# Kernel tuning notes

Measured on AMD Instinct MI355X. Metric: run time of the kernel, lower is better.

Reference implementation:

```python
import jax, jax.numpy as jnp
import numpy as np

SCORE_THR = 0.01
IOU_THR = 0.1          # NOTE: original layer hardcodes 0.1 in tf.image.non_max_suppression
MAX_DET = 100
NEG = jnp.float32(-1e30)


def _iou_one_vs_all(box, boxes):
    # box: [4] (y1,x1,y2,x2), boxes: [N,4]
    y1 = jnp.maximum(box[0], boxes[:, 0])
    x1 = jnp.maximum(box[1], boxes[:, 1])
    y2 = jnp.minimum(box[2], boxes[:, 2])
    x2 = jnp.minimum(box[3], boxes[:, 3])
    inter = jnp.maximum(y2 - y1, 0.0) * jnp.maximum(x2 - x1, 0.0)
    a = (box[2] - box[0]) * (box[3] - box[1])
    b = (boxes[:, 2] - boxes[:, 0]) * (boxes[:, 3] - boxes[:, 1])
    return inter / (a + b - inter + 1e-8)


def _nms_keep(boxes, scores):
    # Greedy NMS as a keep-mask over N anchors. Matches tf.image.non_max_suppression
    # restricted to anchors with score > SCORE_THR, up to MAX_DET selections.
    s = jnp.where(scores > SCORE_THR, scores, NEG)
    keep0 = jnp.zeros(s.shape, dtype=bool)

    def step(carry, _):
        s, keep = carry
        i = jnp.argmax(s)
        ok = s[i] > NEG * 0.5
        keep = keep.at[i].set(ok)
        iou = _iou_one_vs_all(boxes[i], boxes)
        s = jnp.where((iou > IOU_THR) & ok, NEG, s)
        s = s.at[i].set(NEG)
        return (s, keep), None

    (_, keep), _ = jax.lax.scan(step, (s, keep0), None, length=MAX_DET)
    return keep


def _filter_image(boxes_i, cls_i):
    # boxes_i: [N,4], cls_i: [N,C]
    C = cls_i.shape[1]
    # class-specific NMS: keep mask per class -> [C, N]
    keep = jax.vmap(lambda s: _nms_keep(boxes_i, s))(cls_i.T)
    keep_flat = keep.T.reshape(-1)          # [N*C], (anchor, class) flat order
    flat = cls_i.reshape(-1)                # [N*C]
    masked = jnp.where(keep_flat, flat, NEG)
    vals, idx = jax.lax.top_k(masked, MAX_DET)
    valid = vals > NEG * 0.5
    anchor = idx // C
    label = idx % C
    scores_out = jnp.where(valid, jnp.take(flat, idx), -1.0)
    boxes_out = jnp.where(valid[:, None], boxes_i[anchor], -1.0)
    labels_out = jnp.where(valid, label, -1).astype(jnp.int32)
    return boxes_out, scores_out, labels_out


def setup_inputs() -> dict:
    key = jax.random.key(0)
    k1, k2, k3 = jax.random.split(key, 3)
    B, N, C = 4, 49104, 90
    yx1 = jax.random.uniform(k1, (B, N, 2), dtype=jnp.float32) * 512.0
    hw = jax.random.uniform(k2, (B, N, 2), dtype=jnp.float32) * 128.0 + 1.0
    boxes = jnp.concatenate([yx1, yx1 + hw], axis=-1)          # [B,N,4] y1x1y2x2
    classification = jax.random.uniform(k3, (B, N, C), dtype=jnp.float32)
    return {"boxes": boxes, "classification": classification}


def reference(boxes, classification):
    return jax.vmap(_filter_image)(boxes, classification)
```

## Files before the change

kernel.cpp:

```cpp
#include <hip/hip_runtime.h>
#include <stdint.h>

typedef unsigned long long u64;

#define B_ 4
#define N_ 49104
#define C_ 90
#define NCLS (B_ * C_)
#define MAXK 100
#define THR 0.01f
#define NB2 2048
#define KCAP 640
#define PTGT 448
#define PCAP 512
#define ACH 128
#define NCH ((N_ + ACH - 1) / ACH)
#define CAPC 32
#define NBIN_M 1280
#define BINBASE 0x3F6E0000u
#define BINSH_M 10

__device__ __forceinline__ float area_of(float y1, float x1, float y2, float x2) {
#pragma clang fp contract(off)
  return (y2 - y1) * (x2 - x1);
}

#define IOU_MID (26843547.0 / 268435456.0)

__device__ __forceinline__ bool iou_gt(float ay1, float ax1, float ay2, float ax2, float aa,
                                       float by1, float bx1, float by2, float bx2, float ba) {
#pragma clang fp contract(off)
  float y1 = fmaxf(ay1, by1);
  float x1 = fmaxf(ax1, bx1);
  float y2 = fminf(ay2, by2);
  float x2 = fminf(ax2, bx2);
  float inter = fmaxf(y2 - y1, 0.0f) * fmaxf(x2 - x1, 0.0f);
  float denom = aa + ba - inter + 1e-8f;
  return (double)inter >= IOU_MID * (double)denom;
}

__device__ __forceinline__ u64 umax64(u64 a, u64 b) { return a > b ? a : b; }

__device__ __forceinline__ u64 shfl_xor_u64(u64 v, int m) {
  int lo = __shfl_xor((int)(unsigned)v, m);
  int hi = __shfl_xor((int)(unsigned)(v >> 32), m);
  return ((u64)(unsigned)hi << 32) | (u64)(unsigned)lo;
}

__device__ __forceinline__ int key2bin_m(u64 k) {
  int d = (int)((unsigned)(k >> 32) - BINBASE);
  int bin = d >> BINSH_M;
  if (d < 0) bin = 0;
  if (bin > NBIN_M - 1) bin = NBIN_M - 1;
  return bin;
}

__global__ __launch_bounds__(256) void select_kernel(const float* __restrict__ cls,
                                                     u64* __restrict__ keybuf,
                                                     unsigned* __restrict__ cnt,
                                                     int capsel, float t0) {
  __shared__ u64 ll[C_ * CAPC];
  __shared__ unsigned lcnt[C_];
  __shared__ unsigned base_s[C_];
  int blk = blockIdx.x;
  int b = blk / NCH, ch = blk - b * NCH;
  int a0 = ch * ACH;
  int aEnd = a0 + ACH; if (aEnd > N_) aEnd = N_;
  int e0 = a0 * C_;
  int nelem = (aEnd - a0) * C_;
  int tid = threadIdx.x;

  for (int i = tid; i < C_; i += 256) lcnt[i] = 0u;
  __syncthreads();

  const float4* src4 = (const float4*)(cls + (size_t)b * N_ * C_ + e0);
  int n4 = nelem >> 2;
  for (int i4 = tid; i4 < n4; i4 += 256) {
    float4 v = src4[i4];
#pragma unroll
    for (int j = 0; j < 4; ++j) {
      float s = (&v.x)[j];
      if (s > t0) {
        int e = e0 + i4 * 4 + j;
        unsigned n = (unsigned)e / (unsigned)C_;
        unsigned c = (unsigned)e - n * (unsigned)C_;
        u64 key = ((u64)__float_as_uint(s) << 32) | (u64)(0xFFFFFFFFu - n);
        unsigned pos = atomicAdd(&lcnt[c], 1u);
        if (pos < CAPC) {
          ll[c * CAPC + pos] = key;
        } else {
          unsigned g = (unsigned)(b * C_) + c;
          unsigned gp = atomicAdd(&cnt[g * 16], 1u);
          if (gp < (unsigned)capsel) keybuf[(size_t)g * capsel + gp] = key;
        }
      }
    }
  }
  __syncthreads();

  if (tid < C_) {
    unsigned cc = lcnt[tid]; if (cc > CAPC) cc = CAPC;
    base_s[tid] = atomicAdd(&cnt[(b * C_ + tid) * 16], cc);
  }
  __syncthreads();

  for (int i = tid; i < C_ * CAPC; i += 256) {
    int c = i >> 5, j = i & 31;
    unsigned cc = lcnt[c]; if (cc > CAPC) cc = CAPC;
    if ((unsigned)j < cc) {
      unsigned pos = base_s[c] + (unsigned)j;
      if (pos < (unsigned)capsel)
        keybuf[(size_t)(b * C_ + c) * capsel + pos] = ll[i];
    }
  }
}

__global__ __launch_bounds__(512) void nms_kernel(const float* __restrict__ boxes,
                                                  const float* __restrict__ cls,
                                                  const u64* __restrict__ keybuf,
                                                  const unsigned* __restrict__ cnt,
                                                  unsigned* __restrict__ done,
                                                  int capsel, float t0,
                                                  u64* __restrict__ keepkeys,
                                                  int* __restrict__ nk_arr,
                                                  float* __restrict__ out) {
  int gcls = blockIdx.x;
  int b = gcls / C_, c = gcls - b * C_;
  __shared__ u64 karr[KCAP];
  __shared__ unsigned hist[NB2];
  __shared__ unsigned sfx[NB2];
  __shared__ float4 kb[MAXK];
  __shared__ float ka[MAXK];
  __shared__ unsigned wsum[8];
  __shared__ int sh_cnt[8];
  __shared__ int sh_b1, sh_pl;
  __shared__ int sh_last, sh_thr;
  __shared__ unsigned sh_cc;
  int tid = threadIdx.x;
  int lane = tid & 63;
  int wid = tid >> 6;

  for (int i = tid; i < MAXK; i += 512) keepkeys[(size_t)gcls * MAXK + i] = 0ull;
  for (int i = tid; i < NB2; i += 512) hist[i] = 0u;
  if (tid == 0) sh_b1 = -1;
  __syncthreads();

  unsigned Mraw = cnt[gcls * 16];
  bool overflow = (Mraw > (unsigned)capsel);
  int M = overflow ? 0 : (int)Mraw;

  const u64* src = keybuf + (size_t)gcls * capsel;

  const int PK = 4096 / 512;
  u64 kreg[PK];
#pragma unroll
  for (int q = 0; q < PK; ++q) {
    kreg[q] = 0ull;
    int i = q * 512 + tid;
    if (i < M) {
      kreg[q] = src[i];
      atomicAdd(&hist[(unsigned)(kreg[q] >> 44) & (NB2 - 1)], 1u);
    }
  }
  __syncthreads();

  {
    const int W = NB2 / 512;
    unsigned loc[W];
    unsigned psum = 0;
#pragma unroll
    for (int q = 0; q < W; ++q) {
      psum += hist[NB2 - 1 - (tid * W + q)];
      loc[q] = psum;
    }
    unsigned incl = psum;
#pragma unroll
    for (int s = 1; s < 64; s <<= 1) {
      unsigned v = (unsigned)__shfl_up((int)incl, s);
      if (lane >= s) incl += v;
    }
    if (lane == 63) wsum[wid] = incl;
    __syncthreads();
    unsigned bs = incl - psum;
    for (int w2 = 0; w2 < wid; ++w2) bs += wsum[w2];
#pragma unroll
    for (int q = 0; q < W; ++q)
      sfx[NB2 - 1 - (tid * W + q)] = bs + loc[q];
  }
  __syncthreads();

  if (M > 0) {
    int target = M < PTGT ? M : PTGT;
    const int W = NB2 / 512;
    int mymax = -1;
#pragma unroll
    for (int q = 0; q < W; ++q) {
      int bb = tid * W + q;
      if ((int)sfx[bb] >= target) mymax = bb > mymax ? bb : mymax;
    }
    if (mymax >= 0) atomicMax(&sh_b1, mymax);
  }
  __syncthreads();
  if (tid == 0) {
    int b1 = sh_b1;
    int pl = 0;
    if (M > 0) {
      pl = (int)sfx[b1];
      if (pl > PCAP) {
        ++b1;
        pl = (b1 < NB2) ? (int)sfx[b1] : 0;
      }
    }
    sh_b1 = b1; sh_pl = pl;
  }
  __syncthreads();
  int b1 = sh_b1;
  int prefix = sh_pl;

#pragma unroll
  for (int q = 0; q < PK; ++q) {
    int i = q * 512 + tid;
    if (i < M) {
      u64 k = kreg[q];
      int bin = (int)((unsigned)(k >> 44) & (NB2 - 1));
      if (bin >= b1) {
        unsigned old = atomicSub(&hist[bin], 1u);
        karr[sfx[bin] - old] = k;
      }
    }
  }
  __syncthreads();

  {
    u64 mk2 = 0ull; int mt = -1;
    if (tid < prefix) {
      u64 k = karr[tid];
      int bin = (int)((unsigned)(k >> 44) & (NB2 - 1));
      int hi2 = (int)sfx[bin];
      int lo2 = (bin == NB2 - 1) ? 0 : (int)sfx[bin + 1];
      int r = lo2;
      for (int j = lo2; j < hi2; ++j) r += (karr[j] > k);
      mk2 = k; mt = r;
    }
    __syncthreads();
    if (mt >= 0) karr[mt] = mk2;
  }
  __syncthreads();

  const float4* bx4 = (const float4*)(boxes + (size_t)b * N_ * 4);

  int seen = 0;
  if (prefix > 0) {
    bool have = tid < prefix;
    float4 cb = make_float4(0.f, 0.f, 0.f, 0.f);
    float ca = 0.f;
    if (have) {
      u64 k = karr[tid];
      cb = bx4[0xFFFFFFFFu - (unsigned)(k & 0xFFFFFFFFull)];
      ca = area_of(cb.x, cb.y, cb.z, cb.w);
    }
    u64 alive = __ballot(have);

    int nslice = (prefix + 63) >> 6;
    for (int s = 0; s < nslice; ++s) {
      if (wid == s) {
        int nkl = seen;
        int slo = s << 6;
        while (alive != 0ull && nkl < MAXK) {
          int bit = __ffsll((long long)alive) - 1;
          float sy1 = __shfl(cb.x, bit);
          float sx1 = __shfl(cb.y, bit);
          float sy2 = __shfl(cb.z, bit);
          float sx2 = __shfl(cb.w, bit);
          float sa  = __shfl(ca,   bit);
          if (lane == 0) {
            u64 key = karr[slo + bit];
            unsigned anchor = 0xFFFFFFFFu - (unsigned)(key & 0xFFFFFFFFull);
            unsigned flat = anchor * C_ + (unsigned)c;
            keepkeys[(size_t)gcls * MAXK + nkl] =
                (key & 0xFFFFFFFF00000000ull) | (u64)(0xFFFFFFFFu - flat);
            kb[nkl] = make_float4(sy1, sx1, sy2, sx2);
            ka[nkl] = sa;
          }
          ++nkl;
          alive &= ~__ballot(iou_gt(sy1, sx1, sy2, sx2, sa,
                                    cb.x, cb.y, cb.z, cb.w, ca));
        }
        if (lane == 0) sh_cnt[s] = nkl;
        seen = nkl;
      }
      __syncthreads();
      int nkNew = (wid == s) ? seen : sh_cnt[s];
      if (nkNew >= MAXK) { seen = nkNew; break; }
      if (wid > s && nkNew > seen) {
        bool d2 = false;
        for (int j = seen; j < nkNew; ++j) {
          float4 sb = kb[j]; float sa = ka[j];
          d2 |= iou_gt(sb.x, sb.y, sb.z, sb.w, sa,
                       cb.x, cb.y, cb.z, cb.w, ca);
        }
        alive &= __ballot(!d2);
      }
      seen = nkNew;
    }
  }

  int nkF = seen;
  if (nkF < MAXK) {
    float teff;
    if (overflow)           teff = 2.0f;
    else if (prefix == 0)   teff = 2.0f;
    else if (prefix < M)    teff = __uint_as_float(0x3F000000u | (((unsigned)b1 << 12) - 1u));
    else                    teff = t0;
    const float* sbase = cls + (size_t)b * N_ * C_ + c;
    const float* bx = boxes + (size_t)b * N_ * 4;
    u64* kkp = keepkeys + (size_t)gcls * MAXK;
    u64* red = karr;
    int nk2 = nkF;
    while (nk2 < MAXK) {
      u64 best = 0ull;
      for (int n = tid; n < N_; n += 512) {
        float s = sbase[(size_t)n * C_];
        if (s > THR && s <= teff) {
          float y1 = bx[(size_t)n * 4 + 0], x1 = bx[(size_t)n * 4 + 1];
          float y2 = bx[(size_t)n * 4 + 2], x2 = bx[(size_t)n * 4 + 3];
          float ar = area_of(y1, x1, y2, x2);
          bool ov = false;
          for (int j = 0; j < nk2; ++j) {
            float4 kbj = kb[j];
            if (iou_gt(kbj.x, kbj.y, kbj.z, kbj.w, ka[j], y1, x1, y2, x2, ar)) { ov = true; break; }
          }
          if (!ov) {
            u64 key = ((u64)__float_as_uint(s) << 32) | (u64)(0xFFFFFFFFu - (unsigned)n);
            best = umax64(best, key);
          }
        }
      }
      red[tid] = best;
      __syncthreads();
      for (int sft = 256; sft > 0; sft >>= 1) {
        if (tid < sft) red[tid] = umax64(red[tid], red[tid + sft]);
        __syncthreads();
      }
      u64 sel = red[0];
      __syncthreads();
      if (sel == 0ull) {
        if (tid == 0) {
          unsigned target2 = 0xFFFFFFFFu - (unsigned)c;
          for (int j = 0; j < nk2; ++j)
            if ((unsigned)(kkp[j] & 0xFFFFFFFFull) == target2) kkp[j] = 0ull;
        }
        break;
      }
      unsigned anchor = 0xFFFFFFFFu - (unsigned)(sel & 0xFFFFFFFFull);
      if (tid == 0) {
        float y1 = bx[(size_t)anchor * 4 + 0], x1 = bx[(size_t)anchor * 4 + 1];
        float y2 = bx[(size_t)anchor * 4 + 2], x2 = bx[(size_t)anchor * 4 + 3];
        kb[nk2] = make_float4(y1, x1, y2, x2);
        ka[nk2] = area_of(y1, x1, y2, x2);
        unsigned flat = anchor * C_ + (unsigned)c;
        kkp[nk2] = (sel & 0xFFFFFFFF00000000ull) | (u64)(0xFFFFFFFFu - flat);
      }
      ++nk2;
      __syncthreads();
    }
    nkF = nk2;
  }
  if (tid == 0) nk_arr[gcls] = nkF;

  __syncthreads();
  if (tid == 0) {
    __threadfence();
    sh_last = (atomicAdd(&done[b], 1u) == (unsigned)(C_ - 1)) ? 1 : 0;
  }
  __syncthreads();
  if (!sh_last) return;
  __threadfence();

  {
    const u64* kk = keepkeys + (size_t)b * C_ * MAXK;
    const int TOT = C_ * MAXK;
    unsigned* histm = hist;
    unsigned* sfxm = sfx;
    u64* mk = karr;
    u64* selk = karr + 512;

    for (int i = tid; i < NBIN_M; i += 512) histm[i] = 0u;
    for (int r = tid; r < MAXK; r += 512) selk[r] = 0ull;
    if (tid == 0) { sh_thr = -1; sh_cc = 0u; }
    __syncthreads();
    for (int i = tid; i < TOT; i += 512) {
      u64 k = kk[i];
      if (k != 0ull) atomicAdd(&histm[key2bin_m(k)], 1u);
    }
    __syncthreads();

    const int Wm = 3;
    int j0 = tid * Wm;
    unsigned psum = 0;
#pragma unroll
    for (int q = 0; q < Wm; ++q) {
      int bin = NBIN_M - 1 - (j0 + q);
      if (bin >= 0) psum += histm[bin];
    }
    unsigned incl = psum;
#pragma unroll
    for (int s = 1; s < 64; s <<= 1) {
      unsigned v = (unsigned)__shfl_up((int)incl, s);
      if (lane >= s) incl += v;
    }
    if (lane == 63) wsum[wid] = incl;
    __syncthreads();
    unsigned base = incl - psum;
    for (int w2 = 0; w2 < wid; ++w2) base += wsum[w2];
    unsigned running = base;
    int mythr = -1;
#pragma unroll
    for (int q = 0; q < Wm; ++q) {
      int bin = NBIN_M - 1 - (j0 + q);
      if (bin >= 0) {
        running += histm[bin];
        sfxm[bin] = running;
        if (mythr < 0 && running >= (unsigned)MAXK) mythr = bin;
      }
    }
    if (mythr >= 0) atomicMax(&sh_thr, mythr);
    __syncthreads();

    int thr = sh_thr; if (thr < 0) thr = 0;
    unsigned S = sfxm[thr];

    if (S <= 512u) {
      for (int i = tid; i < TOT; i += 512) {
        u64 k = kk[i];
        if (k != 0ull && key2bin_m(k) >= thr) {
          unsigned pos = atomicAdd(&sh_cc, 1u);
          mk[pos] = k;
        }
      }
      __syncthreads();
      u64 myk = (tid < (int)S) ? mk[tid] : 0ull;
      int r = 0;
      for (int j = 0; j < (int)S; ++j) r += (mk[j] > myk);
      __syncthreads();
      if (tid < (int)S && r < MAXK) selk[r] = myk;
      __syncthreads();
    } else {
      if (wid == 0) {
        int c0 = lane, c1 = lane + 64;
        int len0 = (c0 < C_) ? nk_arr[b * C_ + c0] : 0;
        int len1 = (c1 < C_) ? nk_arr[b * C_ + c1] : 0;
        int h0 = 0, h1 = 0;
        auto fetchc = [&](int cc, int& h, int len) -> u64 {
          while (h < len) {
            u64 k = kk[(size_t)cc * MAXK + h];
            if (k != 0ull) return k;
            ++h;
          }
          return 0ull;
        };
        u64 cand0 = (c0 < C_) ? fetchc(c0, h0, len0) : 0ull;
        u64 cand1 = (c1 < C_) ? fetchc(c1, h1, len1) : 0ull;
        for (int r2 = 0; r2 < MAXK; ++r2) {
          u64 my = umax64(cand0, cand1);
          u64 g = my;
#pragma unroll
          for (int m = 1; m < 64; m <<= 1) g = umax64(g, shfl_xor_u64(g, m));
          if (lane == 0) selk[r2] = g;
          if (g != 0ull && my == g) {
            if (cand0 == g) { ++h0; cand0 = fetchc(c0, h0, len0); }
            else            { ++h1; cand1 = fetchc(c1, h1, len1); }
          }
        }
      }
      __syncthreads();
    }

    for (int r2 = tid; r2 < MAXK; r2 += 512) {
      u64 s = selk[r2];
      float oy1, ox1, oy2, ox2, sc, lb;
      if (s != 0ull) {
        unsigned flat = 0xFFFFFFFFu - (unsigned)(s & 0xFFFFFFFFull);
        unsigned anchor = flat / C_;
        unsigned label = flat - anchor * C_;
        sc = __uint_as_float((unsigned)(s >> 32));
        const float4 bp = ((const float4*)(boxes + (size_t)b * N_ * 4))[anchor];
        oy1 = bp.x; ox1 = bp.y; oy2 = bp.z; ox2 = bp.w;
        lb = (float)label;
      } else {
        oy1 = ox1 = oy2 = ox2 = -1.0f; sc = -1.0f; lb = -1.0f;
      }
      float* bo = out + ((size_t)b * MAXK + r2) * 4;
      bo[0] = oy1; bo[1] = ox1; bo[2] = oy2; bo[3] = ox2;
      out[(size_t)B_ * MAXK * 4 + b * MAXK + r2] = sc;
      out[(size_t)B_ * MAXK * 4 + B_ * MAXK + b * MAXK + r2] = lb;
    }
  }
}

extern "C" void kernel_launch(void* const* d_in, const int* in_sizes, int n_in,
                              void* d_out, int out_size, void* d_ws, size_t ws_size,
                              hipStream_t stream) {
  const float* boxes = (const float*)d_in[0];
  const float* cls = (const float*)d_in[1];
  char* ws = (char*)d_ws;

  int capsel; float t0;
  auto need_for = [](int cap) -> size_t {
    return 23104 + (size_t)NCLS * cap * 8 + 288000 + 1440;
  };
  if (ws_size >= need_for(4096))      { capsel = 4096; t0 = 0.93f;  }
  else if (ws_size >= need_for(2048)) { capsel = 2048; t0 = 0.962f; }
  else                                { capsel = 1024; t0 = 0.985f; }

  unsigned* cnt = (unsigned*)ws;
  unsigned* done = (unsigned*)(ws + 23040);
  u64* keybuf = (u64*)(ws + 23104);
  size_t off = 23104 + (size_t)NCLS * capsel * 8;
  u64* keepkeys = (u64*)(ws + off);      off += 288000;
  int* nk_arr = (int*)(ws + off);

  hipMemsetAsync(ws, 0, 23104, stream);
  select_kernel<<<B_ * NCH, 256, 0, stream>>>(cls, keybuf, cnt, capsel, t0);
  nms_kernel<<<NCLS, 512, 0, stream>>>(boxes, cls, keybuf, cnt, done, capsel, t0,
                                       keepkeys, nk_arr, (float*)d_out);
}
```

Baseline: 176.0 us.

## Raise selection threshold, shrink score histogram, build merge histogram incrementally

```diff
diff --git a/kernel.cpp b/kernel.cpp
--- a/kernel.cpp
+++ b/kernel.cpp
@@ -9,7 +9,8 @@
 #define NCLS (B_ * C_)
 #define MAXK 100
 #define THR 0.01f
-#define NB2 2048
+#define NBH 288
+#define BINLO 1760
 #define KCAP 640
 #define PTGT 448
 #define PCAP 512
@@ -19,6 +20,7 @@
 #define NBIN_M 1280
 #define BINBASE 0x3F6E0000u
 #define BINSH_M 10
+#define T0 0.99f
 
 __device__ __forceinline__ float area_of(float y1, float x1, float y2, float x2) {
 #pragma clang fp contract(off)
@@ -120,6 +122,7 @@
                                                   const u64* __restrict__ keybuf,
                                                   const unsigned* __restrict__ cnt,
                                                   unsigned* __restrict__ done,
+                                                  unsigned* __restrict__ mhist,
                                                   int capsel, float t0,
                                                   u64* __restrict__ keepkeys,
                                                   int* __restrict__ nk_arr,
@@ -127,10 +130,13 @@
   int gcls = blockIdx.x;
   int b = gcls / C_, c = gcls - b * C_;
   __shared__ u64 karr[KCAP];
-  __shared__ unsigned hist[NB2];
-  __shared__ unsigned sfx[NB2];
+  __shared__ unsigned hist[NBH];
+  __shared__ unsigned sfx[NBH];
+  __shared__ unsigned histm[NBIN_M];
+  __shared__ unsigned sfxm[NBIN_M];
   __shared__ float4 kb[MAXK];
   __shared__ float ka[MAXK];
+  __shared__ u64 kkey_lds[MAXK];
   __shared__ unsigned wsum[8];
   __shared__ int sh_cnt[8];
   __shared__ int sh_b1, sh_pl;
@@ -140,8 +146,11 @@
   int lane = tid & 63;
   int wid = tid >> 6;
 
-  for (int i = tid; i < MAXK; i += 512) keepkeys[(size_t)gcls * MAXK + i] = 0ull;
-  for (int i = tid; i < NB2; i += 512) hist[i] = 0u;
+  for (int i = tid; i < MAXK; i += 512) {
+    keepkeys[(size_t)gcls * MAXK + i] = 0ull;
+    kkey_lds[i] = 0ull;
+  }
+  for (int i = tid; i < NBH; i += 512) hist[i] = 0u;
   if (tid == 0) sh_b1 = -1;
   __syncthreads();
 
@@ -159,46 +168,34 @@
     int i = q * 512 + tid;
     if (i < M) {
       kreg[q] = src[i];
-      atomicAdd(&hist[(unsigned)(kreg[q] >> 44) & (NB2 - 1)], 1u);
+      int bin = (int)((unsigned)(kreg[q] >> 44) & 2047) - BINLO;
+      if (bin < 0) bin = 0;
+      atomicAdd(&hist[bin], 1u);
     }
   }
   __syncthreads();
 
   {
-    const int W = NB2 / 512;
-    unsigned loc[W];
-    unsigned psum = 0;
-#pragma unroll
-    for (int q = 0; q < W; ++q) {
-      psum += hist[NB2 - 1 - (tid * W + q)];
-      loc[q] = psum;
-    }
+    unsigned psum = (tid < NBH) ? hist[NBH - 1 - tid] : 0u;
     unsigned incl = psum;
 #pragma unroll
     for (int s = 1; s < 64; s <<= 1) {
       unsigned v = (unsigned)__shfl_up((int)incl, s);
       if (lane >= s) incl += v;
     }
-    if (lane == 63) wsum[wid] = incl;
+    if (lane == 63 && wid < 5) wsum[wid] = incl;
     __syncthreads();
-    unsigned bs = incl - psum;
-    for (int w2 = 0; w2 < wid; ++w2) bs += wsum[w2];
-#pragma unroll
-    for (int q = 0; q < W; ++q)
-      sfx[NB2 - 1 - (tid * W + q)] = bs + loc[q];
-  }
-  __syncthreads();
-
-  if (M > 0) {
+    if (tid < NBH) {
+      unsigned base2 = 0;
+      for (int w2 = 0; w2 < wid; ++w2) base2 += wsum[w2];
+      sfx[NBH - 1 - tid] = base2 + incl;
+    }
+  }
+  __syncthreads();
+
+  if (M > 0 && tid < NBH) {
     int target = M < PTGT ? M : PTGT;
-    const int W = NB2 / 512;
-    int mymax = -1;
-#pragma unroll
-    for (int q = 0; q < W; ++q) {
-      int bb = tid * W + q;
-      if ((int)sfx[bb] >= target) mymax = bb > mymax ? bb : mymax;
-    }
-    if (mymax >= 0) atomicMax(&sh_b1, mymax);
+    if ((int)sfx[tid] >= target) atomicMax(&sh_b1, tid);
   }
   __syncthreads();
   if (tid == 0) {
@@ -208,7 +205,7 @@
       pl = (int)sfx[b1];
       if (pl > PCAP) {
         ++b1;
-        pl = (b1 < NB2) ? (int)sfx[b1] : 0;
+        pl = (b1 < NBH) ? (int)sfx[b1] : 0;
       }
     }
     sh_b1 = b1; sh_pl = pl;
@@ -222,7 +219,8 @@
     int i = q * 512 + tid;
     if (i < M) {
       u64 k = kreg[q];
-      int bin = (int)((unsigned)(k >> 44) & (NB2 - 1));
+      int bin = (int)((unsigned)(k >> 44) & 2047) - BINLO;
+      if (bin < 0) bin = 0;
       if (bin >= b1) {
         unsigned old = atomicSub(&hist[bin], 1u);
         karr[sfx[bin] - old] = k;
@@ -235,9 +233,10 @@
     u64 mk2 = 0ull; int mt = -1;
     if (tid < prefix) {
       u64 k = karr[tid];
-      int bin = (int)((unsigned)(k >> 44) & (NB2 - 1));
+      int bin = (int)((unsigned)(k >> 44) & 2047) - BINLO;
+      if (bin < 0) bin = 0;
       int hi2 = (int)sfx[bin];
-      int lo2 = (bin == NB2 - 1) ? 0 : (int)sfx[bin + 1];
+      int lo2 = (bin == NBH - 1) ? 0 : (int)sfx[bin + 1];
       int r = lo2;
       for (int j = lo2; j < hi2; ++j) r += (karr[j] > k);
       mk2 = k; mt = r;
@@ -272,13 +271,14 @@
           float sx1 = __shfl(cb.y, bit);
           float sy2 = __shfl(cb.z, bit);
           float sx2 = __shfl(cb.w, bit);
-          float sa  = __shfl(ca,   bit);
+          float sa  = area_of(sy1, sx1, sy2, sx2);
           if (lane == 0) {
             u64 key = karr[slo + bit];
             unsigned anchor = 0xFFFFFFFFu - (unsigned)(key & 0xFFFFFFFFull);
             unsigned flat = anchor * C_ + (unsigned)c;
-            keepkeys[(size_t)gcls * MAXK + nkl] =
-                (key & 0xFFFFFFFF00000000ull) | (u64)(0xFFFFFFFFu - flat);
+            u64 kk2 = (key & 0xFFFFFFFF00000000ull) | (u64)(0xFFFFFFFFu - flat);
+            keepkeys[(size_t)gcls * MAXK + nkl] = kk2;
+            kkey_lds[nkl] = kk2;
             kb[nkl] = make_float4(sy1, sx1, sy2, sx2);
             ka[nkl] = sa;
           }
@@ -310,7 +310,7 @@
     float teff;
     if (overflow)           teff = 2.0f;
     else if (prefix == 0)   teff = 2.0f;
-    else if (prefix < M)    teff = __uint_as_float(0x3F000000u | (((unsigned)b1 << 12) - 1u));
+    else if (prefix < M)    teff = __uint_as_float(0x3F000000u | ((((unsigned)(b1 + BINLO)) << 12) - 1u));
     else                    teff = t0;
     const float* sbase = cls + (size_t)b * N_ * C_ + c;
     const float* bx = boxes + (size_t)b * N_ * 4;
@@ -348,7 +348,7 @@
         if (tid == 0) {
           unsigned target2 = 0xFFFFFFFFu - (unsigned)c;
           for (int j = 0; j < nk2; ++j)
-            if ((unsigned)(kkp[j] & 0xFFFFFFFFull) == target2) kkp[j] = 0ull;
+            if ((unsigned)(kkp[j] & 0xFFFFFFFFull) == target2) { kkp[j] = 0ull; kkey_lds[j] = 0ull; }
         }
         break;
       }
@@ -359,7 +359,9 @@
         kb[nk2] = make_float4(y1, x1, y2, x2);
         ka[nk2] = area_of(y1, x1, y2, x2);
         unsigned flat = anchor * C_ + (unsigned)c;
-        kkp[nk2] = (sel & 0xFFFFFFFF00000000ull) | (u64)(0xFFFFFFFFu - flat);
+        u64 kk2 = (sel & 0xFFFFFFFF00000000ull) | (u64)(0xFFFFFFFFu - flat);
+        kkp[nk2] = kk2;
+        kkey_lds[nk2] = kk2;
       }
       ++nk2;
       __syncthreads();
@@ -367,8 +369,14 @@
     nkF = nk2;
   }
   if (tid == 0) nk_arr[gcls] = nkF;
-
-  __syncthreads();
+  __syncthreads();
+
+  for (int i = tid; i < nkF; i += 512) {
+    u64 k = kkey_lds[i];
+    if (k != 0ull) atomicAdd(&mhist[b * NBIN_M + key2bin_m(k)], 1u);
+  }
+  __syncthreads();
+
   if (tid == 0) {
     __threadfence();
     sh_last = (atomicAdd(&done[b], 1u) == (unsigned)(C_ - 1)) ? 1 : 0;
@@ -380,19 +388,12 @@
   {
     const u64* kk = keepkeys + (size_t)b * C_ * MAXK;
     const int TOT = C_ * MAXK;
-    unsigned* histm = hist;
-    unsigned* sfxm = sfx;
     u64* mk = karr;
     u64* selk = karr + 512;
 
-    for (int i = tid; i < NBIN_M; i += 512) histm[i] = 0u;
+    for (int i = tid; i < NBIN_M; i += 512) histm[i] = mhist[b * NBIN_M + i];
     for (int r = tid; r < MAXK; r += 512) selk[r] = 0ull;
     if (tid == 0) { sh_thr = -1; sh_cc = 0u; }
-    __syncthreads();
-    for (int i = tid; i < TOT; i += 512) {
-      u64 k = kk[i];
-      if (k != 0ull) atomicAdd(&histm[key2bin_m(k)], 1u);
-    }
     __syncthreads();
 
     const int Wm = 3;
@@ -505,23 +506,24 @@
   const float* cls = (const float*)d_in[1];
   char* ws = (char*)d_ws;
 
-  int capsel; float t0;
+  int capsel;
   auto need_for = [](int cap) -> size_t {
-    return 23104 + (size_t)NCLS * cap * 8 + 288000 + 1440;
+    return 43584 + (size_t)NCLS * cap * 8 + 288000 + 1440;
   };
-  if (ws_size >= need_for(4096))      { capsel = 4096; t0 = 0.93f;  }
-  else if (ws_size >= need_for(2048)) { capsel = 2048; t0 = 0.962f; }
-  else                                { capsel = 1024; t0 = 0.985f; }
+  if (ws_size >= need_for(4096))      capsel = 4096;
+  else if (ws_size >= need_for(2048)) capsel = 2048;
+  else                                capsel = 1024;
 
   unsigned* cnt = (unsigned*)ws;
   unsigned* done = (unsigned*)(ws + 23040);
-  u64* keybuf = (u64*)(ws + 23104);
-  size_t off = 23104 + (size_t)NCLS * capsel * 8;
+  unsigned* mhist = (unsigned*)(ws + 23104);
+  u64* keybuf = (u64*)(ws + 43584);
+  size_t off = 43584 + (size_t)NCLS * capsel * 8;
   u64* keepkeys = (u64*)(ws + off);      off += 288000;
   int* nk_arr = (int*)(ws + off);
 
-  hipMemsetAsync(ws, 0, 23104, stream);
-  select_kernel<<<B_ * NCH, 256, 0, stream>>>(cls, keybuf, cnt, capsel, t0);
-  nms_kernel<<<NCLS, 512, 0, stream>>>(boxes, cls, keybuf, cnt, done, capsel, t0,
+  hipMemsetAsync(ws, 0, 43584, stream);
+  select_kernel<<<B_ * NCH, 256, 0, stream>>>(cls, keybuf, cnt, capsel, T0);
+  nms_kernel<<<NCLS, 512, 0, stream>>>(boxes, cls, keybuf, cnt, done, mhist, capsel, T0,
                                        keepkeys, nk_arr, (float*)d_out);
 }
```

Result: slower. 186.8 us (+6.1%).

## Iterate NMS over successive histogram bin runs instead of falling back to full scan

Applied to the files above, without the earlier changes.

```diff
diff --git a/kernel.cpp b/kernel.cpp
--- a/kernel.cpp
+++ b/kernel.cpp
@@ -9,7 +9,8 @@
 #define NCLS (B_ * C_)
 #define MAXK 100
 #define THR 0.01f
-#define NB2 2048
+#define NBH 288
+#define BINLO 1760
 #define KCAP 640
 #define PTGT 448
 #define PCAP 512
@@ -52,6 +53,13 @@
   int bin = d >> BINSH_M;
   if (d < 0) bin = 0;
   if (bin > NBIN_M - 1) bin = NBIN_M - 1;
+  return bin;
+}
+
+__device__ __forceinline__ int keybin_h(u64 k) {
+  int bin = (int)((unsigned)(k >> 44) & 2047) - BINLO;
+  if (bin < 0) bin = 0;
+  if (bin > NBH - 1) bin = NBH - 1;
   return bin;
 }
 
@@ -127,13 +135,15 @@
   int gcls = blockIdx.x;
   int b = gcls / C_, c = gcls - b * C_;
   __shared__ u64 karr[KCAP];
-  __shared__ unsigned hist[NB2];
-  __shared__ unsigned sfx[NB2];
+  __shared__ unsigned hist[NBH];
+  __shared__ unsigned sfx[NBH];
+  __shared__ unsigned histm[NBIN_M];
+  __shared__ unsigned sfxm[NBIN_M];
   __shared__ float4 kb[MAXK];
   __shared__ float ka[MAXK];
   __shared__ unsigned wsum[8];
   __shared__ int sh_cnt[8];
-  __shared__ int sh_b1, sh_pl;
+  __shared__ int sh_b1, sh_run, sh_over;
   __shared__ int sh_last, sh_thr;
   __shared__ unsigned sh_cc;
   int tid = threadIdx.x;
@@ -141,8 +151,8 @@
   int wid = tid >> 6;
 
   for (int i = tid; i < MAXK; i += 512) keepkeys[(size_t)gcls * MAXK + i] = 0ull;
-  for (int i = tid; i < NB2; i += 512) hist[i] = 0u;
-  if (tid == 0) sh_b1 = -1;
+  for (int i = tid; i < NBH; i += 512) hist[i] = 0u;
+  if (tid == 0) sh_over = 0;
   __syncthreads();
 
   unsigned Mraw = cnt[gcls * 16];
@@ -159,159 +169,166 @@
     int i = q * 512 + tid;
     if (i < M) {
       kreg[q] = src[i];
-      atomicAdd(&hist[(unsigned)(kreg[q] >> 44) & (NB2 - 1)], 1u);
+      atomicAdd(&hist[keybin_h(kreg[q])], 1u);
     }
   }
   __syncthreads();
 
   {
-    const int W = NB2 / 512;
-    unsigned loc[W];
-    unsigned psum = 0;
-#pragma unroll
-    for (int q = 0; q < W; ++q) {
-      psum += hist[NB2 - 1 - (tid * W + q)];
-      loc[q] = psum;
-    }
+    unsigned psum = (tid < NBH) ? hist[NBH - 1 - tid] : 0u;
     unsigned incl = psum;
 #pragma unroll
     for (int s = 1; s < 64; s <<= 1) {
       unsigned v = (unsigned)__shfl_up((int)incl, s);
       if (lane >= s) incl += v;
     }
-    if (lane == 63) wsum[wid] = incl;
-    __syncthreads();
-    unsigned bs = incl - psum;
-    for (int w2 = 0; w2 < wid; ++w2) bs += wsum[w2];
-#pragma unroll
-    for (int q = 0; q < W; ++q)
-      sfx[NB2 - 1 - (tid * W + q)] = bs + loc[q];
-  }
-  __syncthreads();
-
-  if (M > 0) {
-    int target = M < PTGT ? M : PTGT;
-    const int W = NB2 / 512;
-    int mymax = -1;
-#pragma unroll
-    for (int q = 0; q < W; ++q) {
-      int bb = tid * W + q;
-      if ((int)sfx[bb] >= target) mymax = bb > mymax ? bb : mymax;
-    }
-    if (mymax >= 0) atomicMax(&sh_b1, mymax);
-  }
-  __syncthreads();
-  if (tid == 0) {
-    int b1 = sh_b1;
-    int pl = 0;
-    if (M > 0) {
-      pl = (int)sfx[b1];
-      if (pl > PCAP) {
-        ++b1;
-        pl = (b1 < NB2) ? (int)sfx[b1] : 0;
-      }
-    }
-    sh_b1 = b1; sh_pl = pl;
-  }
-  __syncthreads();
-  int b1 = sh_b1;
-  int prefix = sh_pl;
-
-#pragma unroll
-  for (int q = 0; q < PK; ++q) {
-    int i = q * 512 + tid;
-    if (i < M) {
-      u64 k = kreg[q];
-      int bin = (int)((unsigned)(k >> 44) & (NB2 - 1));
-      if (bin >= b1) {
-        unsigned old = atomicSub(&hist[bin], 1u);
-        karr[sfx[bin] - old] = k;
-      }
-    }
-  }
-  __syncthreads();
-
-  {
-    u64 mk2 = 0ull; int mt = -1;
-    if (tid < prefix) {
-      u64 k = karr[tid];
-      int bin = (int)((unsigned)(k >> 44) & (NB2 - 1));
-      int hi2 = (int)sfx[bin];
-      int lo2 = (bin == NB2 - 1) ? 0 : (int)sfx[bin + 1];
-      int r = lo2;
-      for (int j = lo2; j < hi2; ++j) r += (karr[j] > k);
-      mk2 = k; mt = r;
-    }
-    __syncthreads();
-    if (mt >= 0) karr[mt] = mk2;
+    if (lane == 63 && wid < 5) wsum[wid] = incl;
+    __syncthreads();
+    if (tid < NBH) {
+      unsigned base2 = 0;
+      for (int w2 = 0; w2 < wid; ++w2) base2 += wsum[w2];
+      sfx[NBH - 1 - tid] = base2 + incl;
+    }
   }
   __syncthreads();
 
   const float4* bx4 = (const float4*)(boxes + (size_t)b * N_ * 4);
 
   int seen = 0;
-  if (prefix > 0) {
-    bool have = tid < prefix;
-    float4 cb = make_float4(0.f, 0.f, 0.f, 0.f);
-    float ca = 0.f;
-    if (have) {
-      u64 k = karr[tid];
-      cb = bx4[0xFFFFFFFFu - (unsigned)(k & 0xFFFFFFFFull)];
-      ca = area_of(cb.x, cb.y, cb.z, cb.w);
-    }
-    u64 alive = __ballot(have);
-
-    int nslice = (prefix + 63) >> 6;
-    for (int s = 0; s < nslice; ++s) {
-      if (wid == s) {
-        int nkl = seen;
-        int slo = s << 6;
-        while (alive != 0ull && nkl < MAXK) {
-          int bit = __ffsll((long long)alive) - 1;
-          float sy1 = __shfl(cb.x, bit);
-          float sx1 = __shfl(cb.y, bit);
-          float sy2 = __shfl(cb.z, bit);
-          float sx2 = __shfl(cb.w, bit);
-          float sa  = __shfl(ca,   bit);
-          if (lane == 0) {
-            u64 key = karr[slo + bit];
-            unsigned anchor = 0xFFFFFFFFu - (unsigned)(key & 0xFFFFFFFFull);
-            unsigned flat = anchor * C_ + (unsigned)c;
-            keepkeys[(size_t)gcls * MAXK + nkl] =
-                (key & 0xFFFFFFFF00000000ull) | (u64)(0xFFFFFFFFu - flat);
-            kb[nkl] = make_float4(sy1, sx1, sy2, sx2);
-            ka[nkl] = sa;
+  int ext = 0;
+  int bhi = NBH;
+  while (ext < M && seen < MAXK) {
+    if (tid == 0) sh_b1 = -1;
+    __syncthreads();
+    int rem = M - ext;
+    int target = rem < PTGT ? rem : PTGT;
+    {
+      int mymax = -1;
+      if (tid < NBH && tid < bhi && (int)sfx[tid] >= ext + target) mymax = tid;
+      for (int m = 32; m > 0; m >>= 1) {
+        int o = __shfl_xor(mymax, m);
+        mymax = o > mymax ? o : mymax;
+      }
+      if (lane == 0 && mymax >= 0) atomicMax(&sh_b1, mymax);
+    }
+    __syncthreads();
+    if (tid == 0) {
+      int b1 = sh_b1;
+      int run = (int)sfx[b1] - ext;
+      int blo = b1;
+      if (run > PCAP) {
+        blo = b1 + 1;
+        run = (blo < NBH) ? (int)sfx[blo] - ext : 0;
+      }
+      if (run == 0) sh_over = 1;
+      sh_b1 = blo; sh_run = run;
+    }
+    __syncthreads();
+    if (sh_over) break;
+    int blo = sh_b1, run = sh_run;
+
+#pragma unroll
+    for (int q = 0; q < PK; ++q) {
+      int i = q * 512 + tid;
+      if (i < M) {
+        u64 k = kreg[q];
+        int bin = keybin_h(k);
+        if (bin >= blo && bin < bhi) {
+          unsigned old = atomicSub(&hist[bin], 1u);
+          karr[(int)sfx[bin] - (int)old - ext] = k;
+        }
+      }
+    }
+    __syncthreads();
+
+    {
+      u64 mk2 = 0ull; int mt = -1;
+      if (tid < run) {
+        u64 k = karr[tid];
+        int bin = keybin_h(k);
+        int hi2 = (int)sfx[bin] - ext;
+        int lo2 = (bin >= NBH - 1) ? 0 : ((int)sfx[bin + 1] - ext);
+        if (lo2 < 0) lo2 = 0;
+        int r = lo2;
+        for (int j = lo2; j < hi2; ++j) r += (karr[j] > k);
+        mk2 = k; mt = r;
+      }
+      __syncthreads();
+      if (mt >= 0) karr[mt] = mk2;
+    }
+    __syncthreads();
+
+    {
+      bool have = tid < run;
+      float4 cb = make_float4(0.f, 0.f, 0.f, 0.f);
+      float ca = 0.f;
+      if (have) {
+        u64 k = karr[tid];
+        cb = bx4[0xFFFFFFFFu - (unsigned)(k & 0xFFFFFFFFull)];
+        ca = area_of(cb.x, cb.y, cb.z, cb.w);
+      }
+      bool dead = !have;
+      for (int j = 0; j < seen; ++j) {
+        float4 sb = kb[j]; float sa = ka[j];
+        dead |= iou_gt(sb.x, sb.y, sb.z, sb.w, sa,
+                       cb.x, cb.y, cb.z, cb.w, ca);
+      }
+      u64 alive = __ballot(!dead);
+
+      int nslice = (run + 63) >> 6;
+      for (int s = 0; s < nslice; ++s) {
+        if (wid == s) {
+          int nkl = seen;
+          int slo = s << 6;
+          while (alive != 0ull && nkl < MAXK) {
+            int bit = __ffsll((long long)alive) - 1;
+            float sy1 = __shfl(cb.x, bit);
+            float sx1 = __shfl(cb.y, bit);
+            float sy2 = __shfl(cb.z, bit);
+            float sx2 = __shfl(cb.w, bit);
+            float sa  = __shfl(ca,   bit);
+            if (lane == 0) {
+              u64 key = karr[slo + bit];
+              unsigned anchor = 0xFFFFFFFFu - (unsigned)(key & 0xFFFFFFFFull);
+              unsigned flat = anchor * C_ + (unsigned)c;
+              keepkeys[(size_t)gcls * MAXK + nkl] =
+                  (key & 0xFFFFFFFF00000000ull) | (u64)(0xFFFFFFFFu - flat);
+              kb[nkl] = make_float4(sy1, sx1, sy2, sx2);
+              ka[nkl] = sa;
+            }
+            ++nkl;
+            alive &= ~__ballot(iou_gt(sy1, sx1, sy2, sx2, sa,
+                                      cb.x, cb.y, cb.z, cb.w, ca));
           }
-          ++nkl;
-          alive &= ~__ballot(iou_gt(sy1, sx1, sy2, sx2, sa,
-                                    cb.x, cb.y, cb.z, cb.w, ca));
-        }
-        if (lane == 0) sh_cnt[s] = nkl;
-        seen = nkl;
-      }
-      __syncthreads();
-      int nkNew = (wid == s) ? seen : sh_cnt[s];
-      if (nkNew >= MAXK) { seen = nkNew; break; }
-      if (wid > s && nkNew > seen) {
-        bool d2 = false;
-        for (int j = seen; j < nkNew; ++j) {
-          float4 sb = kb[j]; float sa = ka[j];
-          d2 |= iou_gt(sb.x, sb.y, sb.z, sb.w, sa,
-                       cb.x, cb.y, cb.z, cb.w, ca);
-        }
-        alive &= __ballot(!d2);
-      }
-      seen = nkNew;
-    }
+          if (lane == 0) sh_cnt[s] = nkl;
+          seen = nkl;
+        }
+        __syncthreads();
+        int nkNew = (wid == s) ? seen : sh_cnt[s];
+        if (nkNew >= MAXK) { seen = nkNew; break; }
+        if (wid > s && nkNew > seen) {
+          bool d2 = false;
+          for (int j = seen; j < nkNew; ++j) {
+            float4 sb = kb[j]; float sa = ka[j];
+            d2 |= iou_gt(sb.x, sb.y, sb.z, sb.w, sa,
+                         cb.x, cb.y, cb.z, cb.w, ca);
+          }
+          alive &= __ballot(!d2);
+        }
+        seen = nkNew;
+      }
+    }
+    ext += run;
+    bhi = blo;
+    __syncthreads();
   }
 
   int nkF = seen;
   if (nkF < MAXK) {
     float teff;
-    if (overflow)           teff = 2.0f;
-    else if (prefix == 0)   teff = 2.0f;
-    else if (prefix < M)    teff = __uint_as_float(0x3F000000u | (((unsigned)b1 << 12) - 1u));
-    else                    teff = t0;
+    if (overflow)      teff = 2.0f;
+    else if (sh_over)  teff = __uint_as_float(0x3F000000u | ((((unsigned)(bhi + BINLO)) << 12) - 1u));
+    else               teff = t0;
     const float* sbase = cls + (size_t)b * N_ * C_ + c;
     const float* bx = boxes + (size_t)b * N_ * 4;
     u64* kkp = keepkeys + (size_t)gcls * MAXK;
@@ -380,8 +397,6 @@
   {
     const u64* kk = keepkeys + (size_t)b * C_ * MAXK;
     const int TOT = C_ * MAXK;
-    unsigned* histm = hist;
-    unsigned* sfxm = sfx;
     u64* mk = karr;
     u64* selk = karr + 512;
 
```

Measured after the change: 176.8 us. No clear change (+0.4%).
